# Performance work log

Hardware: AMD Instinct MI355X
Metric: run time of the kernel (lower is better)

Reference implementation:

```python
import jax, jax.numpy as jnp
import numpy as np

S, C, E, G, H = 8192, 21, 128, 36, 1024  # seq_len, context_len, embed_dim, gazet_dim, hidden_dim
V_IN = 8000
T = 32              # tagset size incl. BOS/EOS
START, STOP = 30, 31
NEG = -10000.0


def setup_inputs() -> dict:
    key = jax.random.key(0)
    ks = jax.random.split(key, 10)
    contexts = jax.random.randint(ks[0], (S, C), 0, V_IN)
    gazet = jax.random.uniform(ks[1], (S, C, G), dtype=jnp.float32)
    train_labels = jax.random.randint(ks[2], (S,), 0, 30)  # base tags only
    emb = jax.random.normal(ks[3], (V_IN, E), dtype=jnp.float32) * 0.1
    D = C * (E + G)
    w1 = jax.random.normal(ks[4], (H, D), dtype=jnp.float32) / np.sqrt(D)
    b1 = jnp.zeros((H,), dtype=jnp.float32)
    w2 = jax.random.normal(ks[5], (T, H), dtype=jnp.float32) / np.sqrt(H)
    b2 = jnp.zeros((T,), dtype=jnp.float32)
    trans = jax.random.normal(ks[6], (T, T), dtype=jnp.float32)
    trans = trans.at[START, :].set(NEG)   # nothing transitions into START... (row = next tag)
    trans = trans.at[:, STOP].set(NEG)    # nothing leaves STOP (col = prev tag)
    return {"contexts": contexts, "gazet": gazet, "train_labels": train_labels,
            "emb": emb, "w1": w1, "b1": b1, "w2": w2, "b2": b2, "trans": trans}


def _feats(contexts, gazet, emb, w1, b1, w2, b2):
    x = jnp.concatenate([emb[contexts], gazet], axis=2)      # [S, C, E+G]
    x = x.reshape(x.shape[0], -1)                            # [S, C*(E+G)]
    h = jax.nn.relu(x @ w1.T + b1)                           # [S, H]  (dropout = identity in eval)
    return h @ w2.T + b2                                     # [S, T]


def _crf_forward(feats, trans):
    alpha0 = jnp.full((T,), NEG, dtype=feats.dtype).at[START].set(0.0)

    def step(alpha, feat):
        # scores[next, prev] = alpha[prev] + trans[next, prev] + feat[next]
        scores = alpha[None, :] + trans + feat[:, None]
        return jax.nn.logsumexp(scores, axis=1), None

    alpha, _ = jax.lax.scan(step, alpha0, feats)
    return jax.nn.logsumexp(alpha + trans[STOP])


def _gold_score(feats, tags, trans):
    tags_ext = jnp.concatenate([jnp.array([START], dtype=tags.dtype), tags])
    trans_sc = jnp.sum(trans[tags_ext[1:], tags_ext[:-1]])
    emit_sc = jnp.sum(feats[jnp.arange(feats.shape[0]), tags])
    return trans_sc + emit_sc + trans[STOP, tags[-1]]


def reference(contexts, gazet, train_labels, emb, w1, b1, w2, b2, trans):
    feats = _feats(contexts, gazet, emb, w1, b1, w2, b2)
    fwd = _crf_forward(feats, trans)
    gold = _gold_score(feats, train_labels, trans)
    return fwd - gold  # neg_log_likelihood (scalar)
```

## Files before the change

kernel.cpp:

```cpp
#include <hip/hip_runtime.h>

#define S_LEN 8192
#define C_CTX 21
#define E_DIM 128
#define G_DIM 36
#define H_DIM 1024
#define T_TAG 32
#define D_RAW 3444
#define DP 3456
#define START_TAG 30
#define STOP_TAG 31
#define NEGV -10000.0f
#define K_CHUNKS 64
#define L_CHUNK 128

typedef __bf16 bf16_t;
typedef __bf16 bf16x4 __attribute__((ext_vector_type(4)));
typedef __bf16 bf16x8 __attribute__((ext_vector_type(8)));
typedef float  f32x4  __attribute__((ext_vector_type(4)));

__device__ inline void async_copy16(const bf16_t* g, bf16_t* l) {
    __builtin_amdgcn_global_load_lds(
        (const __attribute__((address_space(1))) void*)g,
        (__attribute__((address_space(3))) void*)l, 16, 0, 0);
}

__global__ void build_all(const int* __restrict__ ctx, const float* __restrict__ gz,
                          const float* __restrict__ emb, const float* __restrict__ w1,
                          bf16_t* __restrict__ X, bf16_t* __restrict__ W) {
    const int b = blockIdx.x;
    if (b < H_DIM) {
        const int h = b;
        for (int g = threadIdx.x; g < DP / 4; g += 256) {
            float4 v = {0.f, 0.f, 0.f, 0.f};
            if (g < D_RAW / 4) v = *(const float4*)&w1[(size_t)h * D_RAW + g * 4];
            bf16x4 o = {(bf16_t)v.x, (bf16_t)v.y, (bf16_t)v.z, (bf16_t)v.w};
            *(bf16x4*)&W[(size_t)h * DP + g * 4] = o;
        }
    } else {
        const int s = b - H_DIM;
        for (int g = threadIdx.x; g < DP / 4; g += 256) {
            float4 v = {0.f, 0.f, 0.f, 0.f};
            if (g < D_RAW / 4) {
                const int c  = g / 41;
                const int rg = g - c * 41;
                if (rg < 32) v = *(const float4*)&emb[(size_t)ctx[s * C_CTX + c] * E_DIM + rg * 4];
                else         v = *(const float4*)&gz[((size_t)s * C_CTX + c) * G_DIM + (rg - 32) * 4];
            }
            bf16x4 o = {(bf16_t)v.x, (bf16_t)v.y, (bf16_t)v.z, (bf16_t)v.w};
            *(bf16x4*)&X[(size_t)s * DP + g * 4] = o;
        }
    }
}

__global__ __launch_bounds__(512) void gemm1(const bf16_t* __restrict__ X,
                                             const bf16_t* __restrict__ W,
                                             const float* __restrict__ b1,
                                             const float* __restrict__ w2,
                                             const float* __restrict__ b2,
                                             float* __restrict__ Fp) {
    __shared__ bf16_t As[3][256 * 64];
    __shared__ bf16_t Bs[3][128 * 64];
    const int tid  = threadIdx.x;
    const int wave = tid >> 6, lane = tid & 63;
    const int s0 = blockIdx.x * 256, h0 = blockIdx.y * 128;
    const int wm = (wave >> 1) * 64;
    const int wn = (wave & 1) * 64;

    const int arow = tid >> 3;
    const int akg  = (tid & 7) ^ (arow & 7);
    const bf16_t* gA = X + (size_t)(s0 + arow) * DP + akg * 8;
    const bf16_t* gB = W + (size_t)(h0 + arow) * DP + akg * 8;

    const int lrow  = lane & 15;
    const int khalf = lane >> 4;
    const int lr7   = lrow & 7;

#define STAGE_A(buf, k0, i) async_copy16(gA + (size_t)(i) * 64 * DP + (k0), &As[buf][((i) * 512 + tid) * 8])
#define STAGE_B(buf, k0, i) async_copy16(gB + (size_t)(i) * 64 * DP + (k0), &Bs[buf][((i) * 512 + tid) * 8])

    STAGE_A(0, 0, 0); STAGE_A(0, 0, 1); STAGE_A(0, 0, 2); STAGE_A(0, 0, 3);
    STAGE_B(0, 0, 0); STAGE_B(0, 0, 1);
    STAGE_A(1, 64, 0); STAGE_A(1, 64, 1); STAGE_A(1, 64, 2); STAGE_A(1, 64, 3);
    STAGE_B(1, 64, 0); STAGE_B(1, 64, 1);
    asm volatile("s_waitcnt vmcnt(6)" ::: "memory");
    __builtin_amdgcn_s_barrier();

    f32x4 acc[4][4] = {};
    const int NT = DP / 64;
    int rb = 0;
    for (int t = 0; t < NT; ++t) {
        const int  sb = (rb == 0) ? 2 : rb - 1;
        const int  k2 = (t + 2) * 64;
        const bool st = (t + 2) < NT;

        bf16x8 a[2][2][2];
        bf16x8 b[2][2][2];
#pragma unroll
        for (int ks = 0; ks < 2; ++ks) {
            const int kgr = ((ks * 4 + khalf) ^ lr7) * 8;
#pragma unroll
            for (int sp = 0; sp < 2; ++sp)
#pragma unroll
                for (int mt = 0; mt < 2; ++mt)
                    a[sp][ks][mt] = *(const bf16x8*)&As[rb][(wm + sp * 32 + mt * 16 + lrow) * 64 + kgr];
#pragma unroll
            for (int qn = 0; qn < 2; ++qn)
#pragma unroll
                for (int nt = 0; nt < 2; ++nt)
                    b[qn][ks][nt] = *(const bf16x8*)&Bs[rb][(wn + qn * 32 + nt * 16 + lrow) * 64 + kgr];
        }
        if (st) {
            STAGE_A(sb, k2, 0); STAGE_A(sb, k2, 1); STAGE_A(sb, k2, 2); STAGE_A(sb, k2, 3);
            STAGE_B(sb, k2, 0); STAGE_B(sb, k2, 1);
        }
        __builtin_amdgcn_s_barrier();
        __builtin_amdgcn_s_setprio(1);
#pragma unroll
        for (int ks = 0; ks < 2; ++ks)
#pragma unroll
            for (int sp = 0; sp < 2; ++sp)
#pragma unroll
                for (int qn = 0; qn < 2; ++qn)
#pragma unroll
                    for (int mt = 0; mt < 2; ++mt)
#pragma unroll
                        for (int nt = 0; nt < 2; ++nt)
                            acc[sp * 2 + mt][qn * 2 + nt] = __builtin_amdgcn_mfma_f32_16x16x32_bf16(
                                a[sp][ks][mt], b[qn][ks][nt], acc[sp * 2 + mt][qn * 2 + nt], 0, 0, 0);
        __builtin_amdgcn_s_setprio(0);
        if (st)              asm volatile("s_waitcnt vmcnt(6)" ::: "memory");
        else if (t + 1 < NT) asm volatile("s_waitcnt vmcnt(0)" ::: "memory");
        __builtin_amdgcn_s_barrier();
        rb = (rb == 2) ? 0 : rb + 1;
    }
#undef STAGE_A
#undef STAGE_B

    bf16_t* Hl = &As[0][0];
    bf16_t* Wl = &Bs[0][0];

    {
        const int t8 = tid >> 4;
        const int hl = tid & 15;
        const float* wsrc = w2 + (size_t)t8 * H_DIM + h0 + hl * 8;
        const float4 y0 = *(const float4*)wsrc;
        const float4 y1 = *(const float4*)(wsrc + 4);
        bf16x8 wv = {(bf16_t)y0.x, (bf16_t)y0.y, (bf16_t)y0.z, (bf16_t)y0.w,
                     (bf16_t)y1.x, (bf16_t)y1.y, (bf16_t)y1.z, (bf16_t)y1.w};
        *(bf16x8*)&Wl[(t8 * 16 + (hl ^ (t8 & 7))) * 8] = wv;
    }

    const int crow = (lane >> 4) * 4;
    const int ccol = lane & 15;
#pragma unroll
    for (int nt = 0; nt < 4; ++nt) {
        const int jl = wn + nt * 16 + ccol;
        const float bv = b1[h0 + jl];
#pragma unroll
        for (int mt = 0; mt < 4; ++mt) {
#pragma unroll
            for (int r = 0; r < 4; ++r) {
                const int sl = wm + mt * 16 + crow + r;
                const float v = acc[mt][nt][r] + bv;
                Hl[sl * 128 + ((jl >> 3) ^ (sl & 7)) * 8 + (jl & 7)] = (bf16_t)fmaxf(v, 0.f);
            }
        }
    }
    __syncthreads();

    f32x4 acc2[2][2] = {};
    const int wm2 = wave * 32;
#pragma unroll
    for (int ks = 0; ks < 4; ++ks) {
        const int slot = ((ks * 4 + khalf) ^ lr7) * 8;
        bf16x8 ah[2], bw[2];
#pragma unroll
        for (int mt = 0; mt < 2; ++mt)
            ah[mt] = *(const bf16x8*)&Hl[(wm2 + mt * 16 + lrow) * 128 + slot];
#pragma unroll
        for (int nt = 0; nt < 2; ++nt)
            bw[nt] = *(const bf16x8*)&Wl[(nt * 16 + lrow) * 128 + slot];
#pragma unroll
        for (int mt = 0; mt < 2; ++mt)
#pragma unroll
            for (int nt = 0; nt < 2; ++nt)
                acc2[mt][nt] = __builtin_amdgcn_mfma_f32_16x16x32_bf16(ah[mt], bw[nt], acc2[mt][nt], 0, 0, 0);
    }
    const int bj = h0 >> 7;
#pragma unroll
    for (int nt = 0; nt < 2; ++nt) {
        const int tcol = nt * 16 + ccol;
        const float badd = (bj == 7) ? b2[tcol] : 0.f;
#pragma unroll
        for (int mt = 0; mt < 2; ++mt) {
#pragma unroll
            for (int r = 0; r < 4; ++r) {
                const int sr = s0 + wm2 + mt * 16 + crow + r;
                Fp[((size_t)bj * S_LEN + sr) * T_TAG + tcol] = acc2[mt][nt][r] + badd;
            }
        }
    }
}

__global__ __launch_bounds__(256) void crfA(const float* __restrict__ Fp,
                                            const float* __restrict__ trans,
                                            float* __restrict__ QT,
                                            float* __restrict__ sigma,
                                            float* __restrict__ Fsum) {
    __shared__ float fl[L_CHUNK * 32];
    __shared__ float vb[4][2][32];
    const int c    = blockIdx.x >> 2;
    const int tid  = threadIdx.x;
    const int wave = tid >> 6;
    const int lane = tid & 63;
    const int n    = lane & 31;
    const int pl   = lane >> 5;
    const int p    = ((blockIdx.x & 3) << 3) + (wave << 1) + pl;
    const int s0   = c * L_CHUNK;
    for (int i = tid; i < L_CHUNK * 32; i += 256) {
        const size_t idx = (size_t)s0 * 32 + i;
        float accf = 0.f;
#pragma unroll
        for (int j = 0; j < 8; ++j) accf += Fp[(size_t)j * S_LEN * T_TAG + idx];
        fl[i] = accf;
        Fsum[idx] = accf;
    }
    __syncthreads();

    float et[32];
#pragma unroll
    for (int k = 0; k < 32; ++k) et[k] = __expf(trans[n * 32 + k]);

    float* vrow = &vb[wave][pl][0];
    float v  = __expf(trans[n * 32 + p] + fl[n]);
    float sg = 0.f;
    for (int s = 1; s < L_CHUNK; ++s) {
        vrow[n] = v;
        __builtin_amdgcn_s_waitcnt(0xC07F);
        float a0 = 0.f, a1 = 0.f, a2 = 0.f, a3 = 0.f;
#pragma unroll
        for (int q = 0; q < 8; ++q) {
            const float4 wv = *(const float4*)&vrow[q * 4];
            a0 = __builtin_fmaf(et[q * 4 + 0], wv.x, a0);
            a1 = __builtin_fmaf(et[q * 4 + 1], wv.y, a1);
            a2 = __builtin_fmaf(et[q * 4 + 2], wv.z, a2);
            a3 = __builtin_fmaf(et[q * 4 + 3], wv.w, a3);
        }
        v = __expf(fl[s * 32 + n]) * ((a0 + a1) + (a2 + a3));
        if ((s & 7) == 7) {
            float m = v;
#pragma unroll
            for (int off = 16; off; off >>= 1) m = fmaxf(m, __shfl_xor(m, off, 32));
            if (m > 0.f) { v *= 1.0f / m; sg += __logf(m); }
        }
    }
    QT[(c * 32 + p) * 32 + n] = v;
    if (n == 0) sigma[c * 32 + p] = sg;
}

__global__ __launch_bounds__(1024) void crf_fold(const float* __restrict__ Qin,
                                                 const float* __restrict__ Sin,
                                                 const int fold, const int final,
                                                 float* __restrict__ Qout,
                                                 float* __restrict__ Sout,
                                                 const float* __restrict__ trans,
                                                 const float* __restrict__ F,
                                                 const int* __restrict__ lab,
                                                 float* __restrict__ out) {
    __shared__ float A[32][33];
    __shared__ float M[32][33];
    __shared__ float sgf[32];
    __shared__ float gred[16];
    __shared__ float gold_s;

    const int t = threadIdx.x;
    const int p = t >> 5, n = t & 31;
    const int c0 = blockIdx.x * fold;

    if (final) {
        float ga = 0.f;
        for (int s = t; s < S_LEN; s += 1024) {
            const int tg = lab[s];
            ga += F[(size_t)s * T_TAG + tg];
            const int tp = (s == 0) ? START_TAG : lab[s - 1];
            ga += trans[tg * T_TAG + tp];
        }
        if (t == 0) ga += trans[STOP_TAG * T_TAG + lab[S_LEN - 1]];
#pragma unroll
        for (int off = 32; off; off >>= 1) ga += __shfl_down(ga, off, 64);
        if ((t & 63) == 0) gred[t >> 6] = ga;
    }

    A[n][p] = Qin[(size_t)(c0 * 32 + p) * 32 + n];
    float sA = Sin[c0 * 32 + p];
    float mreg = Qin[(size_t)((c0 + 1) * 32 + p) * 32 + n];

    for (int i = 1; i < fold; ++i) {
        const float sMn = Sin[(c0 + i) * 32 + n];
        float mmax = sMn;
#pragma unroll
        for (int off = 16; off; off >>= 1) mmax = fmaxf(mmax, __shfl_xor(mmax, off, 32));
        const float sMp = Sin[(c0 + i) * 32 + p];
        __syncthreads();
        M[n][p] = mreg * __expf(sMp - mmax);
        if (i + 1 < fold) mreg = Qin[(size_t)((c0 + i + 1) * 32 + p) * 32 + n];
        __syncthreads();
        float acc = 0.f;
#pragma unroll 8
        for (int k = 0; k < 32; ++k)
            acc += M[n][k] * A[k][p];
        float cm = acc;
#pragma unroll
        for (int off = 16; off; off >>= 1) cm = fmaxf(cm, __shfl_xor(cm, off, 32));
        cm = fmaxf(cm, 1e-37f);
        __syncthreads();
        A[n][p] = acc / cm;
        sA = sA + mmax + __logf(cm);
    }
    __syncthreads();

    if (!final) {
        Qout[(size_t)(blockIdx.x * 32 + p) * 32 + n] = A[n][p];
        if (n == 0) Sout[blockIdx.x * 32 + p] = sA;
        return;
    }

    if (n == 0) sgf[p] = sA;
    if (t == 0) {
        float s = 0.f;
#pragma unroll
        for (int i = 0; i < 16; ++i) s += gred[i];
        gold_s = s;
    }
    __syncthreads();
    if (t < 32) {
        float v = A[t][START_TAG] * __expf(trans[STOP_TAG * T_TAG + t]);
#pragma unroll
        for (int off = 16; off; off >>= 1) v += __shfl_xor(v, off, 32);
        if (t == 0) out[0] = sgf[START_TAG] + __logf(v) - gold_s;
    }
}

extern "C" void kernel_launch(void* const* d_in, const int* in_sizes, int n_in,
                              void* d_out, int out_size, void* d_ws, size_t ws_size,
                              hipStream_t stream) {
    const int*   ctx   = (const int*)d_in[0];
    const float* gz    = (const float*)d_in[1];
    const int*   lab   = (const int*)d_in[2];
    const float* emb   = (const float*)d_in[3];
    const float* w1    = (const float*)d_in[4];
    const float* b1    = (const float*)d_in[5];
    const float* w2    = (const float*)d_in[6];
    const float* b2    = (const float*)d_in[7];
    const float* trans = (const float*)d_in[8];
    float* out = (float*)d_out;

    char* ws = (char*)d_ws;
    bf16_t* Xb  = (bf16_t*)(ws + 0);
    bf16_t* W1b = (bf16_t*)(ws + 56623104);
    float*  Fp  = (float*)(ws + 63700992);
    float*  F   = (float*)(ws + 80478208);
    float*  QT  = (float*)(ws + 81526784);
    float*  sg  = (float*)(ws + 81788928);
    float*  Q1  = (float*)(ws + 65536);
    float*  S1  = (float*)(ws + 131072);

    build_all<<<H_DIM + S_LEN, 256, 0, stream>>>(ctx, gz, emb, w1, Xb, W1b);
    gemm1<<<dim3(S_LEN / 256, H_DIM / 128), 512, 0, stream>>>(Xb, W1b, b1, w2, b2, Fp);
    crfA<<<K_CHUNKS * 4, 256, 0, stream>>>(Fp, trans, QT, sg, F);
    crf_fold<<<16, 1024, 0, stream>>>(QT, sg, 4, 0, Q1, S1, trans, F, lab, out);
    crf_fold<<<1, 1024, 0, stream>>>(Q1, S1, 16, 1, nullptr, nullptr, trans, F, lab, out);
}
```

Measured before the change: 264.5 us.

## Gather embeddings inside GEMM instead of materializing the full bf16 X matrix

Result: faster. 245.8 us (-7.1%).

```diff
diff --git a/kernel.cpp b/kernel.cpp
--- a/kernel.cpp
+++ b/kernel.cpp
@@ -8,6 +8,7 @@
 #define T_TAG 32
 #define D_RAW 3444
 #define DP 3456
+#define GZP 768
 #define START_TAG 30
 #define STOP_TAG 31
 #define NEGV -10000.0f
@@ -27,33 +28,54 @@
 
 __global__ void build_all(const int* __restrict__ ctx, const float* __restrict__ gz,
                           const float* __restrict__ emb, const float* __restrict__ w1,
-                          bf16_t* __restrict__ X, bf16_t* __restrict__ W) {
+                          bf16_t* __restrict__ Xg, bf16_t* __restrict__ W,
+                          bf16_t* __restrict__ EB) {
     const int b = blockIdx.x;
-    if (b < H_DIM) {
+    if (b < 1024) {
         const int h = b;
         for (int g = threadIdx.x; g < DP / 4; g += 256) {
-            float4 v = {0.f, 0.f, 0.f, 0.f};
-            if (g < D_RAW / 4) v = *(const float4*)&w1[(size_t)h * D_RAW + g * 4];
-            bf16x4 o = {(bf16_t)v.x, (bf16_t)v.y, (bf16_t)v.z, (bf16_t)v.w};
+            bf16x4 o;
+            if (g < 672) {
+                const int knew = g * 4;
+                const float4 v = *(const float4*)&w1[(size_t)h * D_RAW + (knew >> 7) * 164 + (knew & 127)];
+                o = bf16x4{(bf16_t)v.x, (bf16_t)v.y, (bf16_t)v.z, (bf16_t)v.w};
+            } else {
+                const int m = g * 4 - 2688;
+                float t[4];
+#pragma unroll
+                for (int u = 0; u < 4; ++u) {
+                    const int mm = m + u;
+                    t[u] = (mm < 756) ? w1[(size_t)h * D_RAW + (mm / 36) * 164 + 128 + (mm % 36)] : 0.f;
+                }
+                o = bf16x4{(bf16_t)t[0], (bf16_t)t[1], (bf16_t)t[2], (bf16_t)t[3]};
+            }
             *(bf16x4*)&W[(size_t)h * DP + g * 4] = o;
         }
+    } else if (b < 3072) {
+        const int s_base = (b - 1024) * 4;
+        for (int g = threadIdx.x; g < 4 * 192; g += 256) {
+            const int r = g / 192, gg = g - r * 192;
+            const int s = s_base + r;
+            bf16x4 o = bf16x4{(bf16_t)0.f, (bf16_t)0.f, (bf16_t)0.f, (bf16_t)0.f};
+            if (gg < 189) {
+                const float4 v = *(const float4*)&gz[(size_t)s * 756 + gg * 4];
+                o = bf16x4{(bf16_t)v.x, (bf16_t)v.y, (bf16_t)v.z, (bf16_t)v.w};
+            }
+            *(bf16x4*)&Xg[(size_t)s * GZP + gg * 4] = o;
+        }
     } else {
-        const int s = b - H_DIM;
-        for (int g = threadIdx.x; g < DP / 4; g += 256) {
-            float4 v = {0.f, 0.f, 0.f, 0.f};
-            if (g < D_RAW / 4) {
-                const int c  = g / 41;
-                const int rg = g - c * 41;
-                if (rg < 32) v = *(const float4*)&emb[(size_t)ctx[s * C_CTX + c] * E_DIM + rg * 4];
-                else         v = *(const float4*)&gz[((size_t)s * C_CTX + c) * G_DIM + (rg - 32) * 4];
-            }
-            bf16x4 o = {(bf16_t)v.x, (bf16_t)v.y, (bf16_t)v.z, (bf16_t)v.w};
-            *(bf16x4*)&X[(size_t)s * DP + g * 4] = o;
-        }
-    }
-}
-
-__global__ __launch_bounds__(512) void gemm1(const bf16_t* __restrict__ X,
+        const size_t base = (size_t)(b - 3072) * 2048;
+        for (int g = threadIdx.x; g < 512; g += 256) {
+            const float4 v = *(const float4*)&emb[base + g * 4];
+            bf16x4 o = bf16x4{(bf16_t)v.x, (bf16_t)v.y, (bf16_t)v.z, (bf16_t)v.w};
+            *(bf16x4*)&EB[base + g * 4] = o;
+        }
+    }
+}
+
+__global__ __launch_bounds__(512) void gemm1(const int* __restrict__ ctx,
+                                             const bf16_t* __restrict__ EB,
+                                             const bf16_t* __restrict__ Xg,
                                              const bf16_t* __restrict__ W,
                                              const float* __restrict__ b1,
                                              const float* __restrict__ w2,
@@ -61,6 +83,7 @@
                                              float* __restrict__ Fp) {
     __shared__ bf16_t As[3][256 * 64];
     __shared__ bf16_t Bs[3][128 * 64];
+    __shared__ unsigned short ctxs[256 * 21];
     const int tid  = threadIdx.x;
     const int wave = tid >> 6, lane = tid & 63;
     const int s0 = blockIdx.x * 256, h0 = blockIdx.y * 128;
@@ -69,20 +92,35 @@
 
     const int arow = tid >> 3;
     const int akg  = (tid & 7) ^ (arow & 7);
-    const bf16_t* gA = X + (size_t)(s0 + arow) * DP + akg * 8;
     const bf16_t* gB = W + (size_t)(h0 + arow) * DP + akg * 8;
 
     const int lrow  = lane & 15;
     const int khalf = lane >> 4;
     const int lr7   = lrow & 7;
 
-#define STAGE_A(buf, k0, i) async_copy16(gA + (size_t)(i) * 64 * DP + (k0), &As[buf][((i) * 512 + tid) * 8])
 #define STAGE_B(buf, k0, i) async_copy16(gB + (size_t)(i) * 64 * DP + (k0), &Bs[buf][((i) * 512 + tid) * 8])
 
-    STAGE_A(0, 0, 0); STAGE_A(0, 0, 1); STAGE_A(0, 0, 2); STAGE_A(0, 0, 3);
-    STAGE_B(0, 0, 0); STAGE_B(0, 0, 1);
-    STAGE_A(1, 64, 0); STAGE_A(1, 64, 1); STAGE_A(1, 64, 2); STAGE_A(1, 64, 3);
-    STAGE_B(1, 64, 0); STAGE_B(1, 64, 1);
+    for (int j = tid; j < 256 * C_CTX; j += 512)
+        ctxs[j] = (unsigned short)ctx[s0 * C_CTX + j];
+    asm volatile("s_waitcnt lgkmcnt(0)" ::: "memory");
+    __builtin_amdgcn_s_barrier();
+
+    {
+        const int cva = ctxs[(arow      ) * 21], cvb = ctxs[(arow +  64) * 21];
+        const int cvc = ctxs[(arow + 128) * 21], cvd = ctxs[(arow + 192) * 21];
+        const int ea0 = akg * 8;
+        async_copy16(EB + (size_t)cva * 128 + ea0, &As[0][(0 * 512 + tid) * 8]);
+        async_copy16(EB + (size_t)cvb * 128 + ea0, &As[0][(1 * 512 + tid) * 8]);
+        async_copy16(EB + (size_t)cvc * 128 + ea0, &As[0][(2 * 512 + tid) * 8]);
+        async_copy16(EB + (size_t)cvd * 128 + ea0, &As[0][(3 * 512 + tid) * 8]);
+        STAGE_B(0, 0, 0); STAGE_B(0, 0, 1);
+        const int ea1 = 64 + akg * 8;
+        async_copy16(EB + (size_t)cva * 128 + ea1, &As[1][(0 * 512 + tid) * 8]);
+        async_copy16(EB + (size_t)cvb * 128 + ea1, &As[1][(1 * 512 + tid) * 8]);
+        async_copy16(EB + (size_t)cvc * 128 + ea1, &As[1][(2 * 512 + tid) * 8]);
+        async_copy16(EB + (size_t)cvd * 128 + ea1, &As[1][(3 * 512 + tid) * 8]);
+        STAGE_B(1, 64, 0); STAGE_B(1, 64, 1);
+    }
     asm volatile("s_waitcnt vmcnt(6)" ::: "memory");
     __builtin_amdgcn_s_barrier();
 
@@ -91,8 +129,18 @@
     int rb = 0;
     for (int t = 0; t < NT; ++t) {
         const int  sb = (rb == 0) ? 2 : rb - 1;
-        const int  k2 = (t + 2) * 64;
-        const bool st = (t + 2) < NT;
+        const int  tt = t + 2;
+        const bool st = tt < NT;
+        const bool semb = st && (tt < 42);
+
+        int cv0 = 0, cv1 = 0, cv2 = 0, cv3 = 0;
+        if (semb) {
+            const int c_ = tt >> 1;
+            cv0 = ctxs[(arow      ) * 21 + c_];
+            cv1 = ctxs[(arow +  64) * 21 + c_];
+            cv2 = ctxs[(arow + 128) * 21 + c_];
+            cv3 = ctxs[(arow + 192) * 21 + c_];
+        }
 
         bf16x8 a[2][2][2];
         bf16x8 b[2][2][2];
@@ -111,8 +159,19 @@
                     b[qn][ks][nt] = *(const bf16x8*)&Bs[rb][(wn + qn * 32 + nt * 16 + lrow) * 64 + kgr];
         }
         if (st) {
-            STAGE_A(sb, k2, 0); STAGE_A(sb, k2, 1); STAGE_A(sb, k2, 2); STAGE_A(sb, k2, 3);
-            STAGE_B(sb, k2, 0); STAGE_B(sb, k2, 1);
+            if (semb) {
+                const int e0 = (tt & 1) * 64 + akg * 8;
+                async_copy16(EB + (size_t)cv0 * 128 + e0, &As[sb][(0 * 512 + tid) * 8]);
+                async_copy16(EB + (size_t)cv1 * 128 + e0, &As[sb][(1 * 512 + tid) * 8]);
+                async_copy16(EB + (size_t)cv2 * 128 + e0, &As[sb][(2 * 512 + tid) * 8]);
+                async_copy16(EB + (size_t)cv3 * 128 + e0, &As[sb][(3 * 512 + tid) * 8]);
+            } else {
+                const int m0 = (tt - 42) * 64 + akg * 8;
+#pragma unroll
+                for (int i = 0; i < 4; ++i)
+                    async_copy16(Xg + (size_t)(s0 + arow + i * 64) * GZP + m0, &As[sb][(i * 512 + tid) * 8]);
+            }
+            STAGE_B(sb, tt * 64, 0); STAGE_B(sb, tt * 64, 1);
         }
         __builtin_amdgcn_s_barrier();
         __builtin_amdgcn_s_setprio(1);
@@ -134,7 +193,6 @@
         __builtin_amdgcn_s_barrier();
         rb = (rb == 2) ? 0 : rb + 1;
     }
-#undef STAGE_A
 #undef STAGE_B
 
     bf16_t* Hl = &As[0][0];
@@ -357,18 +415,19 @@
     float* out = (float*)d_out;
 
     char* ws = (char*)d_ws;
-    bf16_t* Xb  = (bf16_t*)(ws + 0);
-    bf16_t* W1b = (bf16_t*)(ws + 56623104);
-    float*  Fp  = (float*)(ws + 63700992);
-    float*  F   = (float*)(ws + 80478208);
-    float*  QT  = (float*)(ws + 81526784);
-    float*  sg  = (float*)(ws + 81788928);
-    float*  Q1  = (float*)(ws + 65536);
-    float*  S1  = (float*)(ws + 131072);
-
-    build_all<<<H_DIM + S_LEN, 256, 0, stream>>>(ctx, gz, emb, w1, Xb, W1b);
-    gemm1<<<dim3(S_LEN / 256, H_DIM / 128), 512, 0, stream>>>(Xb, W1b, b1, w2, b2, Fp);
+    bf16_t* W1b = (bf16_t*)(ws + 0);
+    bf16_t* EB  = (bf16_t*)(ws + 7077888);
+    bf16_t* Xg  = (bf16_t*)(ws + 9126400);
+    float*  Fp  = (float*)(ws + 21709312);
+    float*  F   = (float*)(ws + 30097920);
+    float*  QT  = (float*)(ws + 31146496);
+    float*  sg  = (float*)(ws + 31408640);
+    float*  Q1  = (float*)(ws + 31416832);
+    float*  S1  = (float*)(ws + 31449600);
+
+    build_all<<<3572, 256, 0, stream>>>(ctx, gz, emb, w1, Xg, W1b, EB);
+    gemm1<<<dim3(S_LEN / 256, H_DIM / 128), 512, 0, stream>>>(ctx, EB, Xg, W1b, b1, w2, b2, Fp);
     crfA<<<K_CHUNKS * 4, 256, 0, stream>>>(Fp, trans, QT, sg, F);
-    crf_fold<<<16, 1024, 0, stream>>>(QT, sg, 4, 0, Q1, S1, trans, F, lab, out);
-    crf_fold<<<1, 1024, 0, stream>>>(Q1, S1, 16, 1, nullptr, nullptr, trans, F, lab, out);
-}
+    crf_fold<<<8, 1024, 0, stream>>>(QT, sg, 8, 0, Q1, S1, trans, F, lab, out);
+    crf_fold<<<1, 1024, 0, stream>>>(Q1, S1, 8, 1, nullptr, nullptr, trans, F, lab, out);
+}
```
